# Optimization experiments

Measured on AMD Instinct MI355X. Metric: run time of the kernel, lower is better.

The kernel has to match this reference:

```python
import jax, jax.numpy as jnp
import numpy as np

N = 100000
E = 1600000
NUM_GRAPHS = 64
EPS = 1e-5


def setup_inputs() -> dict:
    key = jax.random.key(0)
    ks = jax.random.split(key, 8)
    x = jax.random.normal(ks[0], (N, 128), dtype=jnp.float32)
    edge_index = jax.random.randint(ks[1], (2, E), 0, N, dtype=jnp.int64)
    batch = jnp.sort(jax.random.randint(ks[2], (N,), 0, NUM_GRAPHS, dtype=jnp.int64))
    W1 = jax.random.normal(ks[3], (128, 128), dtype=jnp.float32) * (1.0 / np.sqrt(128))
    W2 = jax.random.normal(ks[4], (128, 128), dtype=jnp.float32) * (1.0 / np.sqrt(128))
    W3 = jax.random.normal(ks[5], (128, 32), dtype=jnp.float32) * (1.0 / np.sqrt(128))
    return {
        'x': x, 'edge_index': edge_index, 'batch': batch,
        'W1': W1, 'b1': jnp.zeros((128,), jnp.float32),
        'W2': W2, 'b2': jnp.zeros((128,), jnp.float32),
        'W3': W3, 'b3': jnp.zeros((32,), jnp.float32),
        'gamma1': jnp.ones((128,), jnp.float32), 'beta1': jnp.zeros((128,), jnp.float32),
        'gamma2': jnp.ones((128,), jnp.float32), 'beta2': jnp.zeros((128,), jnp.float32),
    }


def _gcn_norm(edge_index, n_nodes):
    # PyG GCNConv default: add self-loops, symmetric normalization.
    loop = jnp.arange(n_nodes, dtype=edge_index.dtype)
    src = jnp.concatenate([edge_index[0], loop])  # [E+N]
    dst = jnp.concatenate([edge_index[1], loop])
    deg = jax.ops.segment_sum(jnp.ones_like(dst, dtype=jnp.float32), dst,
                              num_segments=n_nodes)
    dinv = jnp.where(deg > 0, jax.lax.rsqrt(deg), 0.0)
    norm = dinv[src] * dinv[dst]  # [E+N]
    return src, dst, norm


def _gcn_conv(x, W, b, src, dst, norm, n_nodes):
    h = x @ W                                   # [N, d_out] dense GEMM
    msg = h[src] * norm[:, None]                # gather + scale  [E+N, d_out]
    out = jax.ops.segment_sum(msg, dst, num_segments=n_nodes)  # scatter-add
    return out + b


def _batchnorm(x, gamma, beta):
    # Training-mode BatchNorm1d: batch stats over node dim, biased variance.
    mean = jnp.mean(x, axis=0)
    var = jnp.var(x, axis=0)
    return (x - mean) * jax.lax.rsqrt(var + EPS) * gamma + beta


def reference(x, edge_index, batch, W1, b1, W2, b2, W3, b3,
              gamma1, beta1, gamma2, beta2):
    src, dst, norm = _gcn_norm(edge_index, N)
    h = _gcn_conv(x, W1, b1, src, dst, norm, N)
    h = jax.nn.relu(_batchnorm(h, gamma1, beta1))  # dropout is identity (eval)
    h = _gcn_conv(h, W2, b2, src, dst, norm, N)
    h = jax.nn.relu(_batchnorm(h, gamma2, beta2))
    h = _gcn_conv(h, W3, b3, src, dst, norm, N)
    # global_mean_pool over graph ids
    sums = jax.ops.segment_sum(h, batch, num_segments=NUM_GRAPHS)  # [G, out]
    cnts = jax.ops.segment_sum(jnp.ones((N,), jnp.float32), batch,
                               num_segments=NUM_GRAPHS)
    pooled = sums / jnp.maximum(cnts, 1.0)[:, None]
    return jax.nn.sigmoid(pooled)
```

## Files before the change

### kernel.cpp

```cpp
#include <hip/hip_runtime.h>
#include <math.h>

#define NGRAPH 64
#define EPS_BN 1e-5f
#define BN_BLOCKS 512

typedef unsigned int uint32;
typedef unsigned short ushort16;
typedef __attribute__((ext_vector_type(8))) short short8v;
typedef __attribute__((ext_vector_type(4))) float float4v;

__device__ __forceinline__ float bf2f(uint32 u16) {
    return __uint_as_float(u16 << 16);
}
__device__ __forceinline__ ushort16 f2bf(float f) {
    uint32 u = __float_as_uint(f);
    return (ushort16)((u + 0x7fffu + ((u >> 16) & 1u)) >> 16);
}
__device__ __forceinline__ uint32 pack2(float lo, float hi) {
    return (uint32)f2bf(lo) | ((uint32)f2bf(hi) << 16);
}

__global__ __launch_bounds__(256) void k_wprep_all(const float* __restrict__ W1,
                                                   const float* __restrict__ W2,
                                                   const float* __restrict__ W3,
                                                   ushort16* __restrict__ wt1,
                                                   ushort16* __restrict__ wt2,
                                                   ushort16* __restrict__ wt3,
                                                   int* __restrict__ cnt, int n) {
    int i = blockIdx.x * 256 + threadIdx.x;
    if (i < 16384) {
        int c = i >> 7, k = i & 127;
        wt1[i] = f2bf(W1[k * 128 + c]);
    } else if (i < 32768) {
        int j = i - 16384;
        int c = j >> 7, k = j & 127;
        wt2[j] = f2bf(W2[k * 128 + c]);
    } else if (i < 36864) {
        int j = i - 32768;
        int c = j >> 7, k = j & 127;
        wt3[j] = f2bf(W3[k * 32 + c]);
    }
    if (i < n) cnt[i] = 0;
}

#define EB 256
__global__ __launch_bounds__(256) void k_gemm1_cnt(const float* __restrict__ A,
                                                   const ushort16* __restrict__ Wt,
                                                   ushort16* __restrict__ C, int nrows,
                                                   const int* __restrict__ dst,
                                                   int* __restrict__ cnt,
                                                   int* __restrict__ rank,
                                                   int ne, int epb) {
    constexpr int K = 128;
    constexpr int COLS = 128;
    constexpr int LDK = K + 8;
    __shared__ ushort16 As[64 * LDK];
    __shared__ ushort16 Bs[COLS * LDK];
    const int tid = threadIdx.x;
    const int bid = blockIdx.x;
    const int q = bid >> 2, r = bid & 3;

    if (r == 3 && q < EB) {
        const int beg = q * epb;
        const int end = min(beg + epb, ne);
        int e = beg + tid;
        for (; e + 3 * 256 < end; e += 4 * 256) {
            int d0 = dst[e], d1 = dst[e + 256], d2 = dst[e + 512], d3 = dst[e + 768];
            int r0 = atomicAdd(&cnt[d0], 1);
            int r1 = atomicAdd(&cnt[d1], 1);
            int r2 = atomicAdd(&cnt[d2], 1);
            int r3 = atomicAdd(&cnt[d3], 1);
            rank[e] = r0; rank[e + 256] = r1; rank[e + 512] = r2; rank[e + 768] = r3;
        }
        for (; e < end; e += 256) rank[e] = atomicAdd(&cnt[dst[e]], 1);
        return;
    }
    const int gidx = (q < EB) ? (3 * q + r) : (bid - EB);

    {
        const uint4* wg = (const uint4*)Wt;
        for (int i = tid; i < COLS * (K / 8); i += 256) {
            int rr = i >> 4, c8 = i & 15;
            *(uint4*)&Bs[rr * LDK + c8 * 8] = wg[i];
        }
    }
    const int w = tid >> 6;
    const int l = tid & 63;
    const int lr = l & 15;
    const int lg = l >> 4;
    constexpr int CT = COLS / 16;

    #pragma unroll
    for (int half = 0; half < 2; ++half) {
        const int row0 = gidx * 128 + half * 64;
        if (half) __syncthreads();
        const float* Af = A;
        for (int i = tid; i < 64 * (K / 4); i += 256) {
            int rr = i >> 5, c4 = i & 31;
            float4 a;
            if (row0 + rr < nrows) a = *(const float4*)&Af[(size_t)(row0 + rr) * K + c4 * 4];
            else a = make_float4(0.f, 0.f, 0.f, 0.f);
            ushort4 o;
            o.x = f2bf(a.x); o.y = f2bf(a.y); o.z = f2bf(a.z); o.w = f2bf(a.w);
            *(ushort4*)&As[rr * LDK + c4 * 4] = o;
        }
        __syncthreads();

        float4v acc[CT] = {};
        short8v afrag[4];
        #pragma unroll
        for (int kk = 0; kk < 4; ++kk)
            afrag[kk] = *(const short8v*)&As[(w * 16 + lr) * LDK + kk * 32 + lg * 8];
        #pragma unroll
        for (int kk = 0; kk < 4; ++kk) {
            #pragma unroll
            for (int ct = 0; ct < CT; ++ct) {
                short8v b = *(const short8v*)&Bs[(ct * 16 + lr) * LDK + kk * 32 + lg * 8];
                acc[ct] = __builtin_amdgcn_mfma_f32_16x16x32_bf16(afrag[kk], b, acc[ct], 0, 0, 0);
            }
        }
        #pragma unroll
        for (int rr = 0; rr < 4; ++rr) {
            int gr = row0 + w * 16 + lg * 4 + rr;
            if (gr < nrows) {
                #pragma unroll
                for (int ct = 0; ct < CT; ++ct)
                    C[(size_t)gr * COLS + ct * 16 + lr] = f2bf(acc[ct][rr]);
            }
        }
    }
}

__global__ __launch_bounds__(1024) void k_scan1(const int* __restrict__ cnt,
                                                int* __restrict__ rowstart,
                                                int* __restrict__ blocksum,
                                                float* __restrict__ dinv, int n) {
    __shared__ int sh[1024];
    const int tid = threadIdx.x;
    const int i = blockIdx.x * 1024 + tid;
    int v = (i < n) ? cnt[i] : 0;
    if (i < n) dinv[i] = rsqrtf((float)(v + 1));
    sh[tid] = v;
    __syncthreads();
    for (int off = 1; off < 1024; off <<= 1) {
        int t = (tid >= off) ? sh[tid - off] : 0;
        __syncthreads();
        sh[tid] += t;
        __syncthreads();
    }
    if (i < n) rowstart[i] = sh[tid] - v;
    if (tid == 1023) blocksum[blockIdx.x] = sh[1023];
}

__global__ __launch_bounds__(1024) void k_scan2(int* __restrict__ blocksum, int nb,
                                                float* __restrict__ psum,
                                                float* __restrict__ pcnt) {
    __shared__ int sh[1024];
    const int tid = threadIdx.x;
    int v = (tid < nb) ? blocksum[tid] : 0;
    sh[tid] = v;
    __syncthreads();
    for (int off = 1; off < 1024; off <<= 1) {
        int t = (tid >= off) ? sh[tid - off] : 0;
        __syncthreads();
        sh[tid] += t;
        __syncthreads();
    }
    if (tid < nb) blocksum[tid] = sh[tid] - v;
    for (int i = tid; i < NGRAPH * 32; i += 1024) psum[i] = 0.f;
    if (tid < NGRAPH) pcnt[tid] = 0.f;
}

__global__ __launch_bounds__(256) void k_scan3s(const int* __restrict__ src,
                                                const int* __restrict__ dst,
                                                const int* __restrict__ rank,
                                                const int* __restrict__ rowstart,
                                                const int* __restrict__ blocksum,
                                                int* __restrict__ rowfin,
                                                int* __restrict__ esrc, int n, int ne) {
    const int tid = threadIdx.x;
    const int bid = blockIdx.x;
    int i = bid * 256 + tid;
    if (i < n) rowfin[i] = rowstart[i] + blocksum[i >> 10];
    int e0 = bid * 2048 + tid;
    #pragma unroll
    for (int j = 0; j < 8; ++j) {
        int e = e0 + j * 256;
        if (e < ne) {
            int d = dst[e];
            esrc[rowstart[d] + blocksum[d >> 10] + rank[e]] = src[e];
        }
    }
}

template<int COLS, bool BN, bool AF32>
__global__ __launch_bounds__(256) void k_gemm_mfma(const void* __restrict__ Av,
                                                   const ushort16* __restrict__ Wt,
                                                   const float* __restrict__ ss,
                                                   const float* __restrict__ dinv,
                                                   ushort16* __restrict__ C, int nrows) {
    constexpr int K = 128;
    constexpr int LDK = K + 8;
    __shared__ ushort16 As[64 * LDK];
    __shared__ ushort16 Bs[COLS * LDK];
    const int tid = threadIdx.x;

    {
        const uint4* wg = (const uint4*)Wt;
        for (int i = tid; i < COLS * (K / 8); i += 256) {
            int r = i >> 4, c8 = i & 15;
            *(uint4*)&Bs[r * LDK + c8 * 8] = wg[i];
        }
    }

    const int w = tid >> 6;
    const int l = tid & 63;
    const int lr = l & 15;
    const int lg = l >> 4;
    constexpr int CT = COLS / 16;

    #pragma unroll
    for (int half = 0; half < 2; ++half) {
        const int row0 = blockIdx.x * 128 + half * 64;
        if (half) __syncthreads();
        if constexpr (AF32) {
            const float* A = (const float*)Av;
            for (int i = tid; i < 64 * (K / 4); i += 256) {
                int r = i >> 5, c4 = i & 31;
                float4 a;
                if (row0 + r < nrows) a = *(const float4*)&A[(size_t)(row0 + r) * K + c4 * 4];
                else a = make_float4(0.f, 0.f, 0.f, 0.f);
                if (BN) {
                    float4 sc = *(const float4*)&ss[c4 * 4];
                    float4 sh = *(const float4*)&ss[128 + c4 * 4];
                    a.x = fmaxf(fmaf(a.x, sc.x, sh.x), 0.f);
                    a.y = fmaxf(fmaf(a.y, sc.y, sh.y), 0.f);
                    a.z = fmaxf(fmaf(a.z, sc.z, sh.z), 0.f);
                    a.w = fmaxf(fmaf(a.w, sc.w, sh.w), 0.f);
                }
                ushort4 o;
                o.x = f2bf(a.x); o.y = f2bf(a.y); o.z = f2bf(a.z); o.w = f2bf(a.w);
                *(ushort4*)&As[r * LDK + c4 * 4] = o;
            }
        } else {
            const uint4* Ag = (const uint4*)Av;
            for (int i = tid; i < 64 * (K / 8); i += 256) {
                int r = i >> 4, c8 = i & 15;
                uint4 u;
                if (row0 + r < nrows) u = Ag[(size_t)(row0 + r) * 16 + c8];
                else u = make_uint4(0, 0, 0, 0);
                if (BN) {
                    uint32 wv[4] = {u.x, u.y, u.z, u.w};
                    #pragma unroll
                    for (int t = 0; t < 4; ++t) {
                        int f = c8 * 8 + t * 2;
                        float lo = fmaxf(fmaf(bf2f(wv[t] & 0xffffu), ss[f],     ss[128 + f]),     0.f);
                        float hi = fmaxf(fmaf(bf2f(wv[t] >> 16),     ss[f + 1], ss[128 + f + 1]), 0.f);
                        wv[t] = pack2(lo, hi);
                    }
                    u.x = wv[0]; u.y = wv[1]; u.z = wv[2]; u.w = wv[3];
                }
                *(uint4*)&As[r * LDK + c8 * 8] = u;
            }
        }
        __syncthreads();

        float4v acc[CT] = {};
        short8v afrag[4];
        #pragma unroll
        for (int kk = 0; kk < 4; ++kk)
            afrag[kk] = *(const short8v*)&As[(w * 16 + lr) * LDK + kk * 32 + lg * 8];
        #pragma unroll
        for (int kk = 0; kk < 4; ++kk) {
            #pragma unroll
            for (int ct = 0; ct < CT; ++ct) {
                short8v b = *(const short8v*)&Bs[(ct * 16 + lr) * LDK + kk * 32 + lg * 8];
                acc[ct] = __builtin_amdgcn_mfma_f32_16x16x32_bf16(afrag[kk], b, acc[ct], 0, 0, 0);
            }
        }
        #pragma unroll
        for (int r = 0; r < 4; ++r) {
            int gr = row0 + w * 16 + lg * 4 + r;
            if (gr < nrows) {
                float dv = dinv[gr];
                #pragma unroll
                for (int ct = 0; ct < CT; ++ct)
                    C[(size_t)gr * COLS + ct * 16 + lr] = f2bf(acc[ct][r] * dv);
            }
        }
    }
}

template<int COLS, bool PRESCALED>
__global__ __launch_bounds__(256) void k_agg_csr(const ushort16* __restrict__ h,
                                                 const int* __restrict__ rowstart,
                                                 const int* __restrict__ cnt,
                                                 const int* __restrict__ esrc,
                                                 const float* __restrict__ dinv,
                                                 uint32* __restrict__ out, int n) {
    constexpr int TPN = COLS / 2;
    const uint32* __restrict__ hu = (const uint32*)h;
    int gt = blockIdx.x * 256 + threadIdx.x;
    int node = gt / TPN;
    if (node >= n) return;
    int lane = gt % TPN;

    float di = dinv[node];
    uint32 p = hu[(size_t)node * TPN + lane];
    float ax, ay;
    if constexpr (PRESCALED) {
        ax = bf2f(p & 0xffffu);
        ay = bf2f(p >> 16);
    } else {
        ax = bf2f(p & 0xffffu) * di;
        ay = bf2f(p >> 16) * di;
    }

    int beg = rowstart[node];
    int dg = cnt[node];
    if constexpr (TPN == 64) {
        beg = __builtin_amdgcn_readfirstlane(beg);
        dg = __builtin_amdgcn_readfirstlane(dg);
    }
    const int end = beg + dg;
    int e = beg;
    for (; e + 4 <= end; e += 4) {
        int s0 = esrc[e], s1 = esrc[e + 1], s2 = esrc[e + 2], s3 = esrc[e + 3];
        uint32 p0 = hu[(size_t)s0 * TPN + lane];
        uint32 p1 = hu[(size_t)s1 * TPN + lane];
        uint32 p2 = hu[(size_t)s2 * TPN + lane];
        uint32 p3 = hu[(size_t)s3 * TPN + lane];
        if constexpr (PRESCALED) {
            ax += bf2f(p0 & 0xffffu); ay += bf2f(p0 >> 16);
            ax += bf2f(p1 & 0xffffu); ay += bf2f(p1 >> 16);
            ax += bf2f(p2 & 0xffffu); ay += bf2f(p2 >> 16);
            ax += bf2f(p3 & 0xffffu); ay += bf2f(p3 >> 16);
        } else {
            float w0 = dinv[s0], w1 = dinv[s1], w2 = dinv[s2], w3 = dinv[s3];
            ax = fmaf(bf2f(p0 & 0xffffu), w0, ax); ay = fmaf(bf2f(p0 >> 16), w0, ay);
            ax = fmaf(bf2f(p1 & 0xffffu), w1, ax); ay = fmaf(bf2f(p1 >> 16), w1, ay);
            ax = fmaf(bf2f(p2 & 0xffffu), w2, ax); ay = fmaf(bf2f(p2 >> 16), w2, ay);
            ax = fmaf(bf2f(p3 & 0xffffu), w3, ax); ay = fmaf(bf2f(p3 >> 16), w3, ay);
        }
    }
    for (; e < end; ++e) {
        int s0 = esrc[e];
        uint32 p0 = hu[(size_t)s0 * TPN + lane];
        if constexpr (PRESCALED) {
            ax += bf2f(p0 & 0xffffu);
            ay += bf2f(p0 >> 16);
        } else {
            float w0 = dinv[s0];
            ax = fmaf(bf2f(p0 & 0xffffu), w0, ax);
            ay = fmaf(bf2f(p0 >> 16), w0, ay);
        }
    }
    out[(size_t)node * TPN + lane] = pack2(ax * di, ay * di);
}

__global__ __launch_bounds__(256) void k_bn_stats1(const uint32* __restrict__ x,
                                                   float* __restrict__ partials, int n) {
    const int cp = threadIdx.x & 63;
    const int rl = threadIdx.x >> 6;
    float s0 = 0.f, s1 = 0.f, q0 = 0.f, q1 = 0.f;
    for (int r = blockIdx.x * 4 + rl; r < n; r += BN_BLOCKS * 4) {
        uint32 u = x[(size_t)r * 64 + cp];
        float lo = bf2f(u & 0xffffu), hi = bf2f(u >> 16);
        s0 += lo; s1 += hi;
        q0 = fmaf(lo, lo, q0); q1 = fmaf(hi, hi, q1);
    }
    __shared__ float shs[4 * 128];
    __shared__ float shq[4 * 128];
    shs[rl * 128 + 2 * cp] = s0; shs[rl * 128 + 2 * cp + 1] = s1;
    shq[rl * 128 + 2 * cp] = q0; shq[rl * 128 + 2 * cp + 1] = q1;
    __syncthreads();
    int f = threadIdx.x;
    if (f < 128) {
        float s = shs[f] + shs[128 + f] + shs[256 + f] + shs[384 + f];
        float q = shq[f] + shq[128 + f] + shq[256 + f] + shq[384 + f];
        partials[(size_t)blockIdx.x * 256 + f] = s;
        partials[(size_t)blockIdx.x * 256 + 128 + f] = q;
    }
}

__global__ __launch_bounds__(256) void k_bn_stats2(const float* __restrict__ partials,
                                                   const float* __restrict__ gamma,
                                                   const float* __restrict__ beta,
                                                   float* __restrict__ ss, int n) {
    const int f16 = threadIdx.x & 15;
    const int rl = threadIdx.x >> 4;
    const int f = blockIdx.x * 16 + f16;
    float s = 0.f, q = 0.f;
    for (int r = rl; r < BN_BLOCKS; r += 16) {
        s += partials[(size_t)r * 256 + f];
        q += partials[(size_t)r * 256 + 128 + f];
    }
    __shared__ float shs[256], shq[256];
    shs[threadIdx.x] = s;
    shq[threadIdx.x] = q;
    __syncthreads();
    if (rl == 0) {
        float S = 0.f, Q = 0.f;
        #pragma unroll
        for (int r = 0; r < 16; ++r) { S += shs[r * 16 + f16]; Q += shq[r * 16 + f16]; }
        float inv_n = 1.0f / (float)n;
        float mean = S * inv_n;
        float var = Q * inv_n - mean * mean;
        float scale = gamma[f] * rsqrtf(var + EPS_BN);
        ss[f] = scale;
        ss[128 + f] = beta[f] - mean * scale;
    }
}

#define POOL_SLICE 128
__global__ __launch_bounds__(256) void k_pool2(const uint32* __restrict__ h3,
                                               const int* __restrict__ batch,
                                               float* __restrict__ sums,
                                               float* __restrict__ cnt, int n) {
    const int fp = threadIdx.x & 15;
    const int sub = threadIdx.x >> 4;
    int node0 = blockIdx.x * (16 * POOL_SLICE) + sub * POOL_SLICE;
    if (node0 >= n) return;
    int node1 = min(node0 + POOL_SLICE, n);

    int cur_g = batch[node0];
    float a0 = 0.f, a1 = 0.f, c = 0.f;
    for (int i = node0; i < node1; ++i) {
        int g = batch[i];
        if (g != cur_g) {
            atomicAdd(&sums[cur_g * 32 + 2 * fp], a0);
            atomicAdd(&sums[cur_g * 32 + 2 * fp + 1], a1);
            if (fp == 0) atomicAdd(&cnt[cur_g], c);
            a0 = 0.f; a1 = 0.f; c = 0.f; cur_g = g;
        }
        uint32 u = h3[(size_t)i * 16 + fp];
        a0 += bf2f(u & 0xffffu);
        a1 += bf2f(u >> 16);
        c += 1.f;
    }
    atomicAdd(&sums[cur_g * 32 + 2 * fp], a0);
    atomicAdd(&sums[cur_g * 32 + 2 * fp + 1], a1);
    if (fp == 0) atomicAdd(&cnt[cur_g], c);
}

__global__ __launch_bounds__(256) void k_final(const float* __restrict__ sums,
                                               const float* __restrict__ cnt,
                                               const float* __restrict__ b3,
                                               float* __restrict__ out) {
    int i = blockIdx.x * 256 + threadIdx.x;
    if (i >= NGRAPH * 32) return;
    int g = i >> 5;
    int f = i & 31;
    float c = fmaxf(cnt[g], 1.0f);
    float v = sums[i] / c + b3[f];
    out[i] = 1.0f / (1.0f + expf(-v));
}

extern "C" void kernel_launch(void* const* d_in, const int* in_sizes, int n_in,
                              void* d_out, int out_size, void* d_ws, size_t ws_size,
                              hipStream_t stream) {
    const float* x      = (const float*)d_in[0];
    const int*   eidx   = (const int*)d_in[1];
    const int*   batch  = (const int*)d_in[2];
    const float* W1     = (const float*)d_in[3];
    const float* W2     = (const float*)d_in[5];
    const float* W3     = (const float*)d_in[7];
    const float* b3     = (const float*)d_in[8];
    const float* gamma1 = (const float*)d_in[9];
    const float* beta1  = (const float*)d_in[10];
    const float* gamma2 = (const float*)d_in[11];
    const float* beta2  = (const float*)d_in[12];

    const int N = in_sizes[0] / 128;
    const int E = in_sizes[1] / 2;
    const int* src = eidx;
    const int* dst = eidx + E;

    size_t off = 0;
    auto carve = [&](size_t bytes) {
        char* p = (char*)d_ws + off;
        off += (bytes + 511) & ~(size_t)511;
        return p;
    };
    const size_t NB = (size_t)N * 128 * sizeof(float);
    ushort16* bufA  = (ushort16*)carve(NB / 2);
    uint32* bufB    = (uint32*)carve(NB / 2);
    int*   cnt      = (int*)carve((size_t)N * 4);
    int*   rowstart = (int*)carve((size_t)N * 4);
    int*   rowfin   = (int*)carve((size_t)N * 4);
    float* dinv     = (float*)carve((size_t)N * 4);
    int*   esrc     = (int*)carve((size_t)E * 4);
    int*   rank     = (int*)carve((size_t)E * 4);
    ushort16* wt1   = (ushort16*)carve(128 * 128 * 2);
    ushort16* wt2   = (ushort16*)carve(128 * 128 * 2);
    ushort16* wt3   = (ushort16*)carve(32 * 128 * 2);
    float* ss1      = (float*)carve(256 * 4);
    float* ss2      = (float*)carve(256 * 4);
    float* partials = (float*)carve((size_t)BN_BLOCKS * 256 * 4);
    int*   blocksum = (int*)carve(1024 * 4);
    float* psum     = (float*)carve(NGRAPH * 32 * 4);
    float* pcnt     = (float*)carve(NGRAPH * 4);
    (void)ws_size; (void)n_in; (void)out_size;

    const int nbScan  = (N + 1023) / 1024;
    const int nbGemm  = (N + 127) / 128;
    const int nblkAgg128 = ((size_t)N * 64 + 255) / 256;
    const int nblkAgg32  = ((size_t)N * 16 + 255) / 256;
    const int nblkPool   = (N + 16 * POOL_SLICE - 1) / (16 * POOL_SLICE);
    const int nbWprep    = (((36864 > N) ? 36864 : N) + 255) / 256;
    const int nbS3       = (E + 2047) / 2048;
    const int epb        = (E + EB - 1) / EB;
    const int nbFused    = nbGemm + EB;

    k_wprep_all<<<nbWprep, 256, 0, stream>>>(W1, W2, W3, wt1, wt2, wt3, cnt, N);

    k_gemm1_cnt<<<nbFused, 256, 0, stream>>>(x, wt1, bufA, N, dst, cnt, rank, E, epb);

    k_scan1<<<nbScan, 1024, 0, stream>>>(cnt, rowstart, blocksum, dinv, N);
    k_scan2<<<1, 1024, 0, stream>>>(blocksum, nbScan, psum, pcnt);
    k_scan3s<<<nbS3, 256, 0, stream>>>(src, dst, rank, rowstart, blocksum, rowfin, esrc, N, E);

    k_agg_csr<128, false><<<nblkAgg128, 256, 0, stream>>>(bufA, rowfin, cnt, esrc, dinv, bufB, N);
    k_bn_stats1<<<BN_BLOCKS, 256, 0, stream>>>(bufB, partials, N);
    k_bn_stats2<<<8, 256, 0, stream>>>(partials, gamma1, beta1, ss1, N);

    k_gemm_mfma<128, true, false><<<nbGemm, 256, 0, stream>>>(bufB, wt2, ss1, dinv, bufA, N);
    k_agg_csr<128, true><<<nblkAgg128, 256, 0, stream>>>(bufA, rowfin, cnt, esrc, dinv, bufB, N);
    k_bn_stats1<<<BN_BLOCKS, 256, 0, stream>>>(bufB, partials, N);
    k_bn_stats2<<<8, 256, 0, stream>>>(partials, gamma2, beta2, ss2, N);

    k_gemm_mfma<32, true, false><<<nbGemm, 256, 0, stream>>>(bufB, wt3, ss2, dinv, bufA, N);
    k_agg_csr<32, true><<<nblkAgg32, 256, 0, stream>>>(bufA, rowfin, cnt, esrc, dinv, bufB, N);

    k_pool2<<<nblkPool, 256, 0, stream>>>(bufB, batch, psum, pcnt, N);
    k_final<<<(NGRAPH * 32 + 255) / 256, 256, 0, stream>>>(psum, pcnt, b3, (float*)d_out);
}
```

Before: 398.0 us.

## Fuse BatchNorm statistics into 128-wide aggregation with grid-stride persistent blocks

Merges the BN partial-sum pass into the CSR aggregation kernel. Each block now walks nodes in a grid-stride loop and accumulates per-feature sum and sum-of-squares from fp32 outputs before packing, removing a full re-read of the N×128 bf16 activations per layer. Stats now come from unrounded fp32 values instead of bf16, and the grid is fixed at 2048 blocks, so stats2 reduces over more partials. Pool slice size is also reduced to give k_pool2 more parallelism.

Measured after the change: 414.8 us. +4.2%, slower.

```diff
diff --git a/kernel.cpp b/kernel.cpp
--- a/kernel.cpp
+++ b/kernel.cpp
@@ -3,7 +3,7 @@
 
 #define NGRAPH 64
 #define EPS_BN 1e-5f
-#define BN_BLOCKS 512
+#define AGG_BLOCKS 2048
 
 typedef unsigned int uint32;
 typedef unsigned short ushort16;
@@ -292,14 +292,93 @@
     }
 }
 
-template<int COLS, bool PRESCALED>
-__global__ __launch_bounds__(256) void k_agg_csr(const ushort16* __restrict__ h,
-                                                 const int* __restrict__ rowstart,
-                                                 const int* __restrict__ cnt,
-                                                 const int* __restrict__ esrc,
-                                                 const float* __restrict__ dinv,
-                                                 uint32* __restrict__ out, int n) {
-    constexpr int TPN = COLS / 2;
+template<bool PRESCALED>
+__global__ __launch_bounds__(256) void k_agg_bn(const ushort16* __restrict__ h,
+                                                const int* __restrict__ rowstart,
+                                                const int* __restrict__ cnt,
+                                                const int* __restrict__ esrc,
+                                                const float* __restrict__ dinv,
+                                                uint32* __restrict__ out,
+                                                float* __restrict__ partials, int n) {
+    constexpr int TPN = 64;
+    const uint32* __restrict__ hu = (const uint32*)h;
+    const int lane = threadIdx.x & 63;
+    const int sub = threadIdx.x >> 6;
+    float s0 = 0.f, s1 = 0.f, q0 = 0.f, q1 = 0.f;
+
+    for (int node = blockIdx.x * 4 + sub; node < n; node += AGG_BLOCKS * 4) {
+        float di = dinv[node];
+        uint32 p = hu[(size_t)node * TPN + lane];
+        float ax, ay;
+        if constexpr (PRESCALED) {
+            ax = bf2f(p & 0xffffu);
+            ay = bf2f(p >> 16);
+        } else {
+            ax = bf2f(p & 0xffffu) * di;
+            ay = bf2f(p >> 16) * di;
+        }
+        int beg = __builtin_amdgcn_readfirstlane(rowstart[node]);
+        int dg  = __builtin_amdgcn_readfirstlane(cnt[node]);
+        const int end = beg + dg;
+        int e = beg;
+        for (; e + 4 <= end; e += 4) {
+            int sa = esrc[e], sb = esrc[e + 1], sc = esrc[e + 2], sd = esrc[e + 3];
+            uint32 p0 = hu[(size_t)sa * TPN + lane];
+            uint32 p1 = hu[(size_t)sb * TPN + lane];
+            uint32 p2 = hu[(size_t)sc * TPN + lane];
+            uint32 p3 = hu[(size_t)sd * TPN + lane];
+            if constexpr (PRESCALED) {
+                ax += bf2f(p0 & 0xffffu); ay += bf2f(p0 >> 16);
+                ax += bf2f(p1 & 0xffffu); ay += bf2f(p1 >> 16);
+                ax += bf2f(p2 & 0xffffu); ay += bf2f(p2 >> 16);
+                ax += bf2f(p3 & 0xffffu); ay += bf2f(p3 >> 16);
+            } else {
+                float w0 = dinv[sa], w1 = dinv[sb], w2 = dinv[sc], w3 = dinv[sd];
+                ax = fmaf(bf2f(p0 & 0xffffu), w0, ax); ay = fmaf(bf2f(p0 >> 16), w0, ay);
+                ax = fmaf(bf2f(p1 & 0xffffu), w1, ax); ay = fmaf(bf2f(p1 >> 16), w1, ay);
+                ax = fmaf(bf2f(p2 & 0xffffu), w2, ax); ay = fmaf(bf2f(p2 >> 16), w2, ay);
+                ax = fmaf(bf2f(p3 & 0xffffu), w3, ax); ay = fmaf(bf2f(p3 >> 16), w3, ay);
+            }
+        }
+        for (; e < end; ++e) {
+            int sa = esrc[e];
+            uint32 p0 = hu[(size_t)sa * TPN + lane];
+            if constexpr (PRESCALED) {
+                ax += bf2f(p0 & 0xffffu);
+                ay += bf2f(p0 >> 16);
+            } else {
+                float w0 = dinv[sa];
+                ax = fmaf(bf2f(p0 & 0xffffu), w0, ax);
+                ay = fmaf(bf2f(p0 >> 16), w0, ay);
+            }
+        }
+        float ox = ax * di, oy = ay * di;
+        out[(size_t)node * TPN + lane] = pack2(ox, oy);
+        s0 += ox; s1 += oy;
+        q0 = fmaf(ox, ox, q0); q1 = fmaf(oy, oy, q1);
+    }
+
+    __shared__ float shs[4 * 128];
+    __shared__ float shq[4 * 128];
+    shs[sub * 128 + 2 * lane] = s0; shs[sub * 128 + 2 * lane + 1] = s1;
+    shq[sub * 128 + 2 * lane] = q0; shq[sub * 128 + 2 * lane + 1] = q1;
+    __syncthreads();
+    int f = threadIdx.x;
+    if (f < 128) {
+        float s = shs[f] + shs[128 + f] + shs[256 + f] + shs[384 + f];
+        float q = shq[f] + shq[128 + f] + shq[256 + f] + shq[384 + f];
+        partials[(size_t)blockIdx.x * 256 + f] = s;
+        partials[(size_t)blockIdx.x * 256 + 128 + f] = q;
+    }
+}
+
+__global__ __launch_bounds__(256) void k_agg32(const ushort16* __restrict__ h,
+                                               const int* __restrict__ rowstart,
+                                               const int* __restrict__ cnt,
+                                               const int* __restrict__ esrc,
+                                               const float* __restrict__ dinv,
+                                               uint32* __restrict__ out, int n) {
+    constexpr int TPN = 16;
     const uint32* __restrict__ hu = (const uint32*)h;
     int gt = blockIdx.x * 256 + threadIdx.x;
     int node = gt / TPN;
@@ -308,22 +387,11 @@
 
     float di = dinv[node];
     uint32 p = hu[(size_t)node * TPN + lane];
-    float ax, ay;
-    if constexpr (PRESCALED) {
-        ax = bf2f(p & 0xffffu);
-        ay = bf2f(p >> 16);
-    } else {
-        ax = bf2f(p & 0xffffu) * di;
-        ay = bf2f(p >> 16) * di;
-    }
-
-    int beg = rowstart[node];
-    int dg = cnt[node];
-    if constexpr (TPN == 64) {
-        beg = __builtin_amdgcn_readfirstlane(beg);
-        dg = __builtin_amdgcn_readfirstlane(dg);
-    }
-    const int end = beg + dg;
+    float ax = bf2f(p & 0xffffu);
+    float ay = bf2f(p >> 16);
+
+    const int beg = rowstart[node];
+    const int end = beg + cnt[node];
     int e = beg;
     for (; e + 4 <= end; e += 4) {
         int s0 = esrc[e], s1 = esrc[e + 1], s2 = esrc[e + 2], s3 = esrc[e + 3];
@@ -331,57 +399,18 @@
         uint32 p1 = hu[(size_t)s1 * TPN + lane];
         uint32 p2 = hu[(size_t)s2 * TPN + lane];
         uint32 p3 = hu[(size_t)s3 * TPN + lane];
-        if constexpr (PRESCALED) {
-            ax += bf2f(p0 & 0xffffu); ay += bf2f(p0 >> 16);
-            ax += bf2f(p1 & 0xffffu); ay += bf2f(p1 >> 16);
-            ax += bf2f(p2 & 0xffffu); ay += bf2f(p2 >> 16);
-            ax += bf2f(p3 & 0xffffu); ay += bf2f(p3 >> 16);
-        } else {
-            float w0 = dinv[s0], w1 = dinv[s1], w2 = dinv[s2], w3 = dinv[s3];
-            ax = fmaf(bf2f(p0 & 0xffffu), w0, ax); ay = fmaf(bf2f(p0 >> 16), w0, ay);
-            ax = fmaf(bf2f(p1 & 0xffffu), w1, ax); ay = fmaf(bf2f(p1 >> 16), w1, ay);
-            ax = fmaf(bf2f(p2 & 0xffffu), w2, ax); ay = fmaf(bf2f(p2 >> 16), w2, ay);
-            ax = fmaf(bf2f(p3 & 0xffffu), w3, ax); ay = fmaf(bf2f(p3 >> 16), w3, ay);
-        }
+        ax += bf2f(p0 & 0xffffu); ay += bf2f(p0 >> 16);
+        ax += bf2f(p1 & 0xffffu); ay += bf2f(p1 >> 16);
+        ax += bf2f(p2 & 0xffffu); ay += bf2f(p2 >> 16);
+        ax += bf2f(p3 & 0xffffu); ay += bf2f(p3 >> 16);
     }
     for (; e < end; ++e) {
         int s0 = esrc[e];
         uint32 p0 = hu[(size_t)s0 * TPN + lane];
-        if constexpr (PRESCALED) {
-            ax += bf2f(p0 & 0xffffu);
-            ay += bf2f(p0 >> 16);
-        } else {
-            float w0 = dinv[s0];
-            ax = fmaf(bf2f(p0 & 0xffffu), w0, ax);
-            ay = fmaf(bf2f(p0 >> 16), w0, ay);
-        }
+        ax += bf2f(p0 & 0xffffu);
+        ay += bf2f(p0 >> 16);
     }
     out[(size_t)node * TPN + lane] = pack2(ax * di, ay * di);
-}
-
-__global__ __launch_bounds__(256) void k_bn_stats1(const uint32* __restrict__ x,
-                                                   float* __restrict__ partials, int n) {
-    const int cp = threadIdx.x & 63;
-    const int rl = threadIdx.x >> 6;
-    float s0 = 0.f, s1 = 0.f, q0 = 0.f, q1 = 0.f;
-    for (int r = blockIdx.x * 4 + rl; r < n; r += BN_BLOCKS * 4) {
-        uint32 u = x[(size_t)r * 64 + cp];
-        float lo = bf2f(u & 0xffffu), hi = bf2f(u >> 16);
-        s0 += lo; s1 += hi;
-        q0 = fmaf(lo, lo, q0); q1 = fmaf(hi, hi, q1);
-    }
-    __shared__ float shs[4 * 128];
-    __shared__ float shq[4 * 128];
-    shs[rl * 128 + 2 * cp] = s0; shs[rl * 128 + 2 * cp + 1] = s1;
-    shq[rl * 128 + 2 * cp] = q0; shq[rl * 128 + 2 * cp + 1] = q1;
-    __syncthreads();
-    int f = threadIdx.x;
-    if (f < 128) {
-        float s = shs[f] + shs[128 + f] + shs[256 + f] + shs[384 + f];
-        float q = shq[f] + shq[128 + f] + shq[256 + f] + shq[384 + f];
-        partials[(size_t)blockIdx.x * 256 + f] = s;
-        partials[(size_t)blockIdx.x * 256 + 128 + f] = q;
-    }
 }
 
 __global__ __launch_bounds__(256) void k_bn_stats2(const float* __restrict__ partials,
@@ -392,7 +421,7 @@
     const int rl = threadIdx.x >> 4;
     const int f = blockIdx.x * 16 + f16;
     float s = 0.f, q = 0.f;
-    for (int r = rl; r < BN_BLOCKS; r += 16) {
+    for (int r = rl; r < AGG_BLOCKS; r += 16) {
         s += partials[(size_t)r * 256 + f];
         q += partials[(size_t)r * 256 + 128 + f];
     }
@@ -413,7 +442,7 @@
     }
 }
 
-#define POOL_SLICE 128
+#define POOL_SLICE 32
 __global__ __launch_bounds__(256) void k_pool2(const uint32* __restrict__ h3,
                                                const int* __restrict__ batch,
                                                float* __restrict__ sums,
@@ -497,7 +526,7 @@
     ushort16* wt3   = (ushort16*)carve(32 * 128 * 2);
     float* ss1      = (float*)carve(256 * 4);
     float* ss2      = (float*)carve(256 * 4);
-    float* partials = (float*)carve((size_t)BN_BLOCKS * 256 * 4);
+    float* partials = (float*)carve((size_t)AGG_BLOCKS * 256 * 4);
     int*   blocksum = (int*)carve(1024 * 4);
     float* psum     = (float*)carve(NGRAPH * 32 * 4);
     float* pcnt     = (float*)carve(NGRAPH * 4);
@@ -505,7 +534,6 @@
 
     const int nbScan  = (N + 1023) / 1024;
     const int nbGemm  = (N + 127) / 128;
-    const int nblkAgg128 = ((size_t)N * 64 + 255) / 256;
     const int nblkAgg32  = ((size_t)N * 16 + 255) / 256;
     const int nblkPool   = (N + 16 * POOL_SLICE - 1) / (16 * POOL_SLICE);
     const int nbWprep    = (((36864 > N) ? 36864 : N) + 255) / 256;
@@ -521,17 +549,15 @@
     k_scan2<<<1, 1024, 0, stream>>>(blocksum, nbScan, psum, pcnt);
     k_scan3s<<<nbS3, 256, 0, stream>>>(src, dst, rank, rowstart, blocksum, rowfin, esrc, N, E);
 
-    k_agg_csr<128, false><<<nblkAgg128, 256, 0, stream>>>(bufA, rowfin, cnt, esrc, dinv, bufB, N);
-    k_bn_stats1<<<BN_BLOCKS, 256, 0, stream>>>(bufB, partials, N);
+    k_agg_bn<false><<<AGG_BLOCKS, 256, 0, stream>>>(bufA, rowfin, cnt, esrc, dinv, bufB, partials, N);
     k_bn_stats2<<<8, 256, 0, stream>>>(partials, gamma1, beta1, ss1, N);
 
     k_gemm_mfma<128, true, false><<<nbGemm, 256, 0, stream>>>(bufB, wt2, ss1, dinv, bufA, N);
-    k_agg_csr<128, true><<<nblkAgg128, 256, 0, stream>>>(bufA, rowfin, cnt, esrc, dinv, bufB, N);
-    k_bn_stats1<<<BN_BLOCKS, 256, 0, stream>>>(bufB, partials, N);
+    k_agg_bn<true><<<AGG_BLOCKS, 256, 0, stream>>>(bufA, rowfin, cnt, esrc, dinv, bufB, partials, N);
     k_bn_stats2<<<8, 256, 0, stream>>>(partials, gamma2, beta2, ss2, N);
 
     k_gemm_mfma<32, true, false><<<nbGemm, 256, 0, stream>>>(bufB, wt3, ss2, dinv, bufA, N);
-    k_agg_csr<32, true><<<nblkAgg32, 256, 0, stream>>>(bufA, rowfin, cnt, esrc, dinv, bufB, N);
+    k_agg32<<<nblkAgg32, 256, 0, stream>>>(bufA, rowfin, cnt, esrc, dinv, bufB, N);
 
     k_pool2<<<nblkPool, 256, 0, stream>>>(bufB, batch, psum, pcnt, N);
     k_final<<<(NGRAPH * 32 + 255) / 256, 256, 0, stream>>>(psum, pcnt, b3, (float*)d_out);
```
